# Kernel optimization log

Measured on AMD Instinct MI355X. Metric: run time of the kernel, lower is better.

The kernel has to match this reference:

```python
import jax, jax.numpy as jnp
import numpy as np

# MANO prior contact vertex indices (f1+f2+f3+f4+f5+f0 from CMap_loss3)
_F1 = [697,698,699,700,712,713,714,715,737,738,739,740,741,743,744,745,746,748,749,750,753,754,755,756,757,758,759,760,761,762,763,764,765,766,767,768]
_F2 = [46,47,48,49,164,165,166,167,194,195,223,237,238,280,281,298,301,317,320,323,324,325,326,327,328,329,330,331,332,333,340,341,342,343,344,345,346,347,348,349,350,351,352,353,354,355]
_F3 = [356,357,358,359,375,376,386,387,396,397,402,403,413,429,433,434,435,436,437,438,439,440,441,442,443,444,452,453,454,455,456,459,460,461,462,463,464,465,466,467]
_F4 = [468,469,470,471,484,485,486,496,497,506,507,513,514,524,545,546,547,548,549,550,551,552,553,555,563,564,565,566,567,570,572,573,574,575,576,577,578]
_F5 = [580,581,582,583,600,601,602,614,615,624,625,630,631,641,663,664,665,666,667,668,670,672,680,681,682,683,684,686,687,688,689,690,691,692,693,694,695]
_F0 = [73,96,98,99,772,774,775,777]
PRIOR_IDX = np.array(_F1 + _F2 + _F3 + _F4 + _F5 + _F0, dtype=np.int32)


def _sqdist(a, b):
    # a: [B,N,3], b: [B,M,3] -> squared distances [B,N,M] via ||a||^2+||b||^2-2ab
    a2 = jnp.sum(a * a, -1)          # [B,N]
    b2 = jnp.sum(b * b, -1)          # [B,M]
    ab = jnp.einsum('bnd,bmd->bnm', a, b)
    return jnp.maximum(a2[:, :, None] + b2[:, None, :] - 2.0 * ab, 0.0)


def _knn1(src, trg):
    # nearest neighbor (K=1): squared dists + indices, like pytorch3d knn_points
    d2 = _sqdist(src, trg)           # [B,N,M]
    return jnp.min(d2, -1), jnp.argmin(d2, -1)


def _verts_normals(verts, faces):
    # area-weighted vertex normals (pytorch3d verts_normals_packed)
    v0 = verts[:, faces[:, 0]]       # [B,F,3]
    v1 = verts[:, faces[:, 1]]
    v2 = verts[:, faces[:, 2]]
    fn = jnp.cross(v1 - v0, v2 - v0)
    vn = jnp.zeros_like(verts)
    vn = vn.at[:, faces[:, 0]].add(fn).at[:, faces[:, 1]].add(fn).at[:, faces[:, 2]].add(fn)
    return vn / (jnp.linalg.norm(vn, axis=-1, keepdims=True) + 1e-12)


def setup_inputs() -> dict:
    key = jax.random.key(0)
    ks = jax.random.split(key, 8)
    B, N1, V, F, Z, P = 64, 8192, 778, 1538, 64, 61
    scale = 0.1  # keep points in a 0.1 box so contact thresholds (0.005/0.01) fire
    return {
        'obj_xyz': jax.random.uniform(ks[0], (B, N1, 3), jnp.float32) * scale,
        'recon_xyz': jax.random.uniform(ks[1], (B, V, 3), jnp.float32) * scale,
        'gt_xyz': jax.random.uniform(ks[2], (B, V, 3), jnp.float32) * scale,
        'mean': jax.random.normal(ks[3], (B, Z), jnp.float32),
        'log_var': jax.random.normal(ks[4], (B, Z), jnp.float32),
        'recon_param': jax.random.normal(ks[5], (B, P), jnp.float32),
        'x_param': jax.random.normal(ks[6], (B, P), jnp.float32),
        'faces': jax.random.randint(ks[7], (F, 3), 0, V, jnp.int32),
    }


def reference(obj_xyz, recon_xyz, gt_xyz, mean, log_var, recon_param, x_param, faces):
    B = obj_xyz.shape[0]
    fB = jnp.float32(B)

    # KNN from object points to gt / reconstructed hand (squared dists)
    d_gt, _ = _knn1(obj_xyz, gt_xyz)            # [B,N1]
    d_rec, idx_rec = _knn1(obj_xyz, recon_xyz)  # [B,N1], [B,N1]

    # param loss: MSE sum / B
    param_loss = jnp.sum((recon_param - x_param) ** 2) / fB

    # CVAE loss: chamfer (point_reduction='sum', batch_reduction='mean') + KLD
    d2 = _sqdist(recon_xyz, gt_xyz)             # [B,778,778]
    recon_loss = jnp.mean(jnp.sum(jnp.min(d2, -1), -1)) + jnp.mean(jnp.sum(jnp.min(d2, -2), -1))
    KLD = -0.5 * jnp.sum(1.0 + log_var - mean ** 2 - jnp.exp(log_var)) / fB * 10.0
    cvae_loss = recon_loss + KLD

    # CMap_loss3: obj NN distance to prior hand contact verts, masked by cmap
    cmap = d_rec < 0.01 ** 2                    # [B,N1] bool
    prior = recon_xyz[:, PRIOR_IDX, :]          # [B,222,3]
    obj_CD, _ = _knn1(obj_xyz, prior)           # [B,N1]
    n_points = jnp.sum(cmap).astype(jnp.float32)
    cmap_loss = 3000.0 * jnp.sum(jnp.where(cmap, obj_CD, 0.0)) / (fB * n_points)

    # CMap consistency: contact-map overlap ratio
    recon_cmap = jnp.sqrt(d_rec) < 0.005
    gt_cmap = jnp.sqrt(d_gt) < 0.005
    gt_cnum = jnp.sum(gt_cmap).astype(jnp.float32) + 0.0001
    consistency_loss = -5.0 * jnp.sum(recon_cmap & gt_cmap).astype(jnp.float32) / gt_cnum

    # inter-penetration: gather NN hand verts/normals, sign of dot, masked dist sum
    vn = _verts_normals(recon_xyz, faces)                               # [B,778,3]
    nn_v = jnp.take_along_axis(recon_xyz, idx_rec[..., None], axis=1)   # [B,N1,3]
    nn_n = jnp.take_along_axis(vn, idx_rec[..., None], axis=1)          # [B,N1,3]
    interior = jnp.sum((nn_v - obj_xyz) * nn_n, -1) > 0                 # [B,N1]
    penetr_loss = 100.0 * jnp.sum(jnp.where(interior, d_rec, 0.0)) / fB

    a, b, c, d, e = 1.0, 0.1, 1000.0, 10.0, 10.0
    loss = a * cvae_loss + b * param_loss + c * cmap_loss + d * consistency_loss + e * penetr_loss
    return loss
```

## Files before the change

### kernel.cpp

```cpp
#include <hip/hip_runtime.h>
#include <math.h>

#define NB     64
#define N1V    8192
#define NPTS   (NB * N1V)
#define NV     778
#define NVP    780
#define NQ     195
#define SEG1Q  51
#define NFACE  1538
#define NZ     64
#define NPAR   61
#define NPRIOR 204
#define PPT    8
#define BIAS   0.0625f

#define GT_BLOCKS  256
#define REC_BLOCKS 256
#define CH_BLOCKS  128
#define NRM_BLOCKS 64
#define REC_BASE GT_BLOCKS
#define CH_BASE  (REC_BASE + REC_BLOCKS)
#define NRM_BASE (CH_BASE + CH_BLOCKS)
#define NBLOCKS  (NRM_BASE + NRM_BLOCKS)

#define ACC_OFF   (NB * NVP * 4)
#define FLAGS_OFF (ACC_OFF + 16)
#define NFLAGS    320
#define GC_OFF    (FLAGS_OFF + NFLAGS)

static constexpr int PRIOR_LIST[NPRIOR] = {
  697,698,699,700,712,713,714,715,737,738,739,740,741,743,744,745,746,748,749,750,
  753,754,755,756,757,758,759,760,761,762,763,764,765,766,767,768,
  46,47,48,49,164,165,166,167,194,195,223,237,238,280,281,298,301,317,320,323,
  324,325,326,327,328,329,330,331,332,333,340,341,342,343,344,345,346,347,348,349,
  350,351,352,353,354,355,
  356,357,358,359,375,376,386,387,396,397,402,403,413,429,433,434,435,436,437,438,
  439,440,441,442,443,444,452,453,454,455,456,459,460,461,462,463,464,465,466,467,
  468,469,470,471,484,485,486,496,497,506,507,513,514,524,545,546,547,548,549,550,
  551,552,553,555,563,564,565,566,567,570,572,573,574,575,576,577,578,
  580,581,582,583,600,601,602,614,615,624,625,630,631,641,663,664,665,666,667,668,
  670,672,680,681,682,683,684,686,687,688,689,690,691,692,693,694,695,
  73,96,98,99,772,774,775,777
};

struct PermT { unsigned short v[NV]; };
static constexpr PermT make_perm() {
    PermT t{};
    bool mem[NV] = {};
    for (int i = 0; i < NPRIOR; ++i) mem[PRIOR_LIST[i]] = true;
    int a = 0, b = NPRIOR;
    for (int j = 0; j < NV; ++j) {
        if (mem[j]) t.v[a++] = (unsigned short)j;
        else        t.v[b++] = (unsigned short)j;
    }
    return t;
}
__device__ __constant__ PermT c_perm = make_perm();

struct ScanSh { float4 t[NVP]; float red[4]; };
struct NrmSh  { float x[NV], y[NV], z[NV], vnx[NV], vny[NV], vnz[NV]; };
union ShU { ScanSh scan; NrmSh nrm; };

#define LOAD_PTS(ob)                                                          \
    const float4* ob4 = (const float4*)((ob) + (size_t)tid * 24);             \
    float4 q0 = ob4[0], q1 = ob4[1], q2 = ob4[2],                             \
           q3 = ob4[3], q4 = ob4[4], q5 = ob4[5];                             \
    float px[PPT], py[PPT], pz[PPT];                                          \
    px[0]=q0.x; py[0]=q0.y; pz[0]=q0.z;  px[1]=q0.w; py[1]=q1.x; pz[1]=q1.y;  \
    px[2]=q1.z; py[2]=q1.w; pz[2]=q2.x;  px[3]=q2.y; py[3]=q2.z; pz[3]=q2.w;  \
    px[4]=q3.x; py[4]=q3.y; pz[4]=q3.z;  px[5]=q3.w; py[5]=q4.x; pz[5]=q4.y;  \
    px[6]=q4.z; py[6]=q4.w; pz[6]=q5.x;  px[7]=q5.y; py[7]=q5.z; pz[7]=q5.w;

__device__ __forceinline__ float min3f(float a, float b, float c) {
    return fminf(fminf(a, b), c);
}

__device__ __forceinline__ void spin_wait(unsigned int* f, int tid) {
    if (tid == 0) {
        while (__hip_atomic_load(f, __ATOMIC_ACQUIRE, __HIP_MEMORY_SCOPE_AGENT) == 0u)
            __builtin_amdgcn_s_sleep(2);
    }
    __syncthreads();
}


__global__ __launch_bounds__(256) void k_all(
        const float* __restrict__ obj,   const float* __restrict__ recon,
        const float* __restrict__ gt,    const int*   __restrict__ faces,
        const float* __restrict__ mean,  const float* __restrict__ log_var,
        const float* __restrict__ rp,    const float* __restrict__ xp,
        float4* __restrict__ ws4,        float* __restrict__ acc,
        unsigned int* __restrict__ flags, unsigned char* __restrict__ gcA,
        float* __restrict__ out) {
    __shared__ ShU sh;
    __shared__ unsigned int s_tk;
    __shared__ float s_pk[2];
    int tid = threadIdx.x;
    int blk = blockIdx.x;

    if (blk < GT_BLOCKS) {
        int r = blk, b = r >> 2, chunk = r & 3;
        const float* gb = gt + (size_t)b * NV * 3;
        float4* s_t = sh.scan.t;
        for (int j = tid; j < NVP; j += 256) {
            if (j < NV) {
                float x = gb[3*j], y = gb[3*j+1], z = gb[3*j+2];
                s_t[j] = make_float4(-2.0f*x, -2.0f*y, -2.0f*z, x*x + y*y + z*z);
            } else s_t[j] = make_float4(0.f, 0.f, 0.f, 1e30f);
        }
        if (tid == 0) sh.scan.red[0] = 0.0f;
        __syncthreads();

        const float* ob = obj + ((size_t)b * N1V + (size_t)chunk * 2048) * 3;
        LOAD_PTS(ob)
        float mgt[PPT];
#pragma unroll
        for (int i = 0; i < PPT; ++i) mgt[i] = 3.4e38f;
#pragma unroll 1
        for (int jq = 0; jq < NQ; ++jq) {
            int j = 4 * jq;
            float4 t0 = s_t[j], t1 = s_t[j+1], t2 = s_t[j+2], t3 = s_t[j+3];
#pragma unroll
            for (int i = 0; i < PPT; ++i) {
                float d0 = fmaf(px[i], t0.x, fmaf(py[i], t0.y, fmaf(pz[i], t0.z, t0.w)));
                float d1 = fmaf(px[i], t1.x, fmaf(py[i], t1.y, fmaf(pz[i], t1.z, t1.w)));
                float d2 = fmaf(px[i], t2.x, fmaf(py[i], t2.y, fmaf(pz[i], t2.z, t2.w)));
                float d3 = fmaf(px[i], t3.x, fmaf(py[i], t3.y, fmaf(pz[i], t3.z, t3.w)));
                float u = min3f(d0, d1, d2);
                mgt[i] = min3f(u, d3, mgt[i]);
            }
        }
        float lN_gt = 0.0f;
        unsigned int gcbits = 0;
#pragma unroll
        for (int i = 0; i < PPT; ++i) {
            float a2 = px[i]*px[i] + py[i]*py[i] + pz[i]*pz[i];
            float dgt = fmaxf(a2 + mgt[i], 0.0f);
            if (sqrtf(dgt) < 0.005f) { lN_gt += 1.0f; gcbits |= (1u << i); }
        }
        gcA[(size_t)r * 256 + tid] = (unsigned char)gcbits;
        atomicAdd(&sh.scan.red[0], lN_gt);
        __syncthreads();
        if (tid == 0) {
            __threadfence();
            __hip_atomic_store(&flags[r], 1u, __ATOMIC_RELEASE, __HIP_MEMORY_SCOPE_AGENT);
            atomicAdd(&acc[5], sh.scan.red[0]);
        }
    } else if (blk < CH_BASE) {
        int r = blk - REC_BASE, b = r >> 2, chunk = r & 3;
        const float* rb = recon + (size_t)b * NV * 3;
        float4* s_t = sh.scan.t;
        for (int j = tid; j < NVP; j += 256) {
            if (j < NV) {
                int src = c_perm.v[j];
                float x = rb[3*src], y = rb[3*src+1], z = rb[3*src+2];
                s_t[j] = make_float4(-2.0f*x, -2.0f*y, -2.0f*z, x*x + y*y + z*z + BIAS);
            } else s_t[j] = make_float4(0.f, 0.f, 0.f, 1e30f);
        }
        if (tid < 4) sh.scan.red[tid] = 0.0f;
        __syncthreads();

        const float* ob = obj + ((size_t)b * N1V + (size_t)chunk * 2048) * 3;
        LOAD_PTS(ob)
        float m[PPT];
        int q[PPT];
#pragma unroll
        for (int i = 0; i < PPT; ++i) { m[i] = 3.4e38f; q[i] = 0; }
        float mp[PPT];
#pragma unroll 1
        for (int jq = 0; jq < SEG1Q; ++jq) {
            int j = 4 * jq;
            float4 t0 = s_t[j], t1 = s_t[j+1], t2 = s_t[j+2], t3 = s_t[j+3];
#pragma unroll
            for (int i = 0; i < PPT; ++i) {
                float d0 = fmaf(px[i], t0.x, fmaf(py[i], t0.y, fmaf(pz[i], t0.z, t0.w)));
                float d1 = fmaf(px[i], t1.x, fmaf(py[i], t1.y, fmaf(pz[i], t1.z, t1.w)));
                float d2 = fmaf(px[i], t2.x, fmaf(py[i], t2.y, fmaf(pz[i], t2.z, t2.w)));
                float d3 = fmaf(px[i], t3.x, fmaf(py[i], t3.y, fmaf(pz[i], t3.z, t3.w)));
                float u  = min3f(d0, d1, d2);
                float mn = min3f(u, d3, m[i]);
                q[i] = (mn < m[i]) ? jq : q[i];
                m[i] = mn;
            }
        }
#pragma unroll
        for (int i = 0; i < PPT; ++i) mp[i] = m[i];
#pragma unroll 1
        for (int jq = SEG1Q; jq < NQ; ++jq) {
            int j = 4 * jq;
            float4 t0 = s_t[j], t1 = s_t[j+1], t2 = s_t[j+2], t3 = s_t[j+3];
#pragma unroll
            for (int i = 0; i < PPT; ++i) {
                float d0 = fmaf(px[i], t0.x, fmaf(py[i], t0.y, fmaf(pz[i], t0.z, t0.w)));
                float d1 = fmaf(px[i], t1.x, fmaf(py[i], t1.y, fmaf(pz[i], t1.z, t1.w)));
                float d2 = fmaf(px[i], t2.x, fmaf(py[i], t2.y, fmaf(pz[i], t2.z, t2.w)));
                float d3 = fmaf(px[i], t3.x, fmaf(py[i], t3.y, fmaf(pz[i], t3.z, t3.w)));
                float u  = min3f(d0, d1, d2);
                float mn = min3f(u, d3, m[i]);
                q[i] = (mn < m[i]) ? jq : q[i];
                m[i] = mn;
            }
        }
        float lS_cmap = 0.0f, lN_cmap = 0.0f;
        unsigned int rcbits = 0;
        int js[PPT]; float drecs[PPT];
#pragma unroll
        for (int i = 0; i < PPT; ++i) {
            float a2 = px[i]*px[i] + py[i]*py[i] + pz[i]*pz[i];
            float drec = fmaxf(a2 + (m[i]  - BIAS), 0.0f);
            float dpri = fmaxf(a2 + (mp[i] - BIAS), 0.0f);
            bool cm = drec < 1e-4f;
            bool rc = sqrtf(drec) < 0.005f;
            if (cm) { lS_cmap += dpri; lN_cmap += 1.0f; }
            if (rc) rcbits |= (1u << i);
            int jr = 4 * q[i];
            float4 t0 = s_t[jr], t1 = s_t[jr+1], t2 = s_t[jr+2], t3 = s_t[jr+3];
            float d0 = fmaf(px[i], t0.x, fmaf(py[i], t0.y, fmaf(pz[i], t0.z, t0.w)));
            float d1 = fmaf(px[i], t1.x, fmaf(py[i], t1.y, fmaf(pz[i], t1.z, t1.w)));
            float d2 = fmaf(px[i], t2.x, fmaf(py[i], t2.y, fmaf(pz[i], t2.z, t2.w)));
            float d3 = fmaf(px[i], t3.x, fmaf(py[i], t3.y, fmaf(pz[i], t3.z, t3.w)));
            float mmin = fminf(fminf(d0, d1), fminf(d2, d3));
            int off = (d0 == mmin) ? 0 : ((d1 == mmin) ? 1 : ((d2 == mmin) ? 2 : 3));
            js[i] = jr + off;
            drecs[i] = drec;
        }
        atomicAdd(&sh.scan.red[0], lS_cmap);
        atomicAdd(&sh.scan.red[1], lN_cmap);
        spin_wait(&flags[256 + b], tid);
        spin_wait(&flags[r], tid);
        const float4* nrm4p = ws4 + (size_t)b * NVP;
        float lS_pen = 0.0f;
#pragma unroll
        for (int i = 0; i < PPT; ++i) {
            float4 tS = s_t[js[i]];
            float4 nr = nrm4p[js[i]];
            float ddot = (-0.5f*tS.x - px[i]) * nr.x + (-0.5f*tS.y - py[i]) * nr.y
                       + (-0.5f*tS.z - pz[i]) * nr.z;
            if (ddot > 0.0f) lS_pen += drecs[i];
        }
        unsigned int gcb = gcA[(size_t)r * 256 + tid];
        float lcons = (float)__popc(rcbits & gcb);
        atomicAdd(&sh.scan.red[2], lS_pen);
        atomicAdd(&sh.scan.red[3], lcons);
        __syncthreads();
        if (tid == 0) atomicAdd(&acc[3], sh.scan.red[0]);
        if (tid == 1) atomicAdd(&acc[4], sh.scan.red[1]);
        if (tid == 2) atomicAdd(&acc[7], sh.scan.red[2]);
        if (tid == 3) atomicAdd(&acc[6], sh.scan.red[3]);
    } else if (blk < NRM_BASE) {
        int c   = blk - CH_BASE;
        int b   = c >> 1;
        int dir = c & 1;
        const float* rb = recon + (size_t)b * NV * 3;
        const float* gb = gt    + (size_t)b * NV * 3;
        const float* tb = dir ? rb : gb;
        const float* sb = dir ? gb : rb;
        float4* s_t = sh.scan.t;
        for (int j = tid; j < NVP; j += 256) {
            if (j < NV) {
                float x = tb[3*j], y = tb[3*j+1], z = tb[3*j+2];
                float w = x*x + y*y + z*z;
                if (dir) w += BIAS;
                s_t[j] = make_float4(-2.0f*x, -2.0f*y, -2.0f*z, w);
            } else s_t[j] = make_float4(0.f, 0.f, 0.f, 1e30f);
        }
        if (tid == 0) sh.scan.red[0] = 0.0f;
        __syncthreads();

        const int CPT = 4;
        float sx[CPT], sy[CPT], sz[CPT], a2[CPT], m[CPT];
        bool valid[CPT];
#pragma unroll
        for (int k = 0; k < CPT; ++k) {
            int p = tid + 256 * k;
            valid[k] = (p < NV);
            int pp = valid[k] ? p : 0;
            float x = sb[3*pp], y = sb[3*pp+1], z = sb[3*pp+2];
            float w = x*x + y*y + z*z;
            if (!dir) w += BIAS;
            sx[k] = x; sy[k] = y; sz[k] = z;
            a2[k] = w;
            m[k] = 3.4e38f;
        }
#pragma unroll 1
        for (int j = 0; j < NVP; j += 4) {
            float4 t0 = s_t[j], t1 = s_t[j+1], t2 = s_t[j+2], t3 = s_t[j+3];
#pragma unroll
            for (int k = 0; k < CPT; ++k) {
                float d0 = fmaf(sx[k], t0.x, fmaf(sy[k], t0.y, fmaf(sz[k], t0.z, t0.w)));
                float d1 = fmaf(sx[k], t1.x, fmaf(sy[k], t1.y, fmaf(sz[k], t1.z, t1.w)));
                float d2 = fmaf(sx[k], t2.x, fmaf(sy[k], t2.y, fmaf(sz[k], t2.z, t2.w)));
                float d3 = fmaf(sx[k], t3.x, fmaf(sy[k], t3.y, fmaf(sz[k], t3.z, t3.w)));
                float u = min3f(d0, d1, d2);
                m[k] = min3f(u, d3, m[k]);
            }
        }
        float local = 0.0f;
#pragma unroll
        for (int k = 0; k < CPT; ++k)
            if (valid[k]) local += fmaxf(a2[k] + m[k] - BIAS, 0.0f);
        atomicAdd(&sh.scan.red[0], local);
        __syncthreads();
        if (tid == 0) atomicAdd(&acc[2], sh.scan.red[0]);
    } else {
        int b = blk - NRM_BASE;
        const float* rb = recon + (size_t)b * NV * 3;
        for (int j = tid; j < NV; j += 256) {
            sh.nrm.x[j] = rb[3*j]; sh.nrm.y[j] = rb[3*j+1]; sh.nrm.z[j] = rb[3*j+2];
            sh.nrm.vnx[j] = 0.0f; sh.nrm.vny[j] = 0.0f; sh.nrm.vnz[j] = 0.0f;
        }
        __syncthreads();
        for (int f = tid; f < NFACE; f += 256) {
            int i0 = faces[3*f], i1 = faces[3*f+1], i2 = faces[3*f+2];
            float p0x = sh.nrm.x[i0], p0y = sh.nrm.y[i0], p0z = sh.nrm.z[i0];
            float e1x = sh.nrm.x[i1] - p0x, e1y = sh.nrm.y[i1] - p0y, e1z = sh.nrm.z[i1] - p0z;
            float e2x = sh.nrm.x[i2] - p0x, e2y = sh.nrm.y[i2] - p0y, e2z = sh.nrm.z[i2] - p0z;
            float fx = e1y * e2z - e1z * e2y;
            float fy = e1z * e2x - e1x * e2z;
            float fz = e1x * e2y - e1y * e2x;
            atomicAdd(&sh.nrm.vnx[i0], fx); atomicAdd(&sh.nrm.vny[i0], fy); atomicAdd(&sh.nrm.vnz[i0], fz);
            atomicAdd(&sh.nrm.vnx[i1], fx); atomicAdd(&sh.nrm.vny[i1], fy); atomicAdd(&sh.nrm.vnz[i1], fz);
            atomicAdd(&sh.nrm.vnx[i2], fx); atomicAdd(&sh.nrm.vny[i2], fy); atomicAdd(&sh.nrm.vnz[i2], fz);
        }
        __syncthreads();
        float4* nrm4p = ws4 + (size_t)b * NVP;
        for (int j = tid; j < NVP; j += 256) {
            if (j < NV) {
                int src = c_perm.v[j];
                nrm4p[j] = make_float4(sh.nrm.vnx[src], sh.nrm.vny[src], sh.nrm.vnz[src], 0.0f);
            } else nrm4p[j] = make_float4(0.f, 0.f, 1.f, 0.0f);
        }
        __syncthreads();
        if (tid == 0) {
            __threadfence();
            __hip_atomic_store(&flags[256 + b], 1u, __ATOMIC_RELEASE, __HIP_MEMORY_SCOPE_AGENT);
        }
        if (b == 0) {
            if (tid < 2) s_pk[tid] = 0.0f;
            __syncthreads();
            float s_param = 0.0f, s_kld = 0.0f;
            for (int i = tid; i < NB * NPAR; i += 256) {
                float d = rp[i] - xp[i];
                s_param += d * d;
            }
            for (int i = tid; i < NB * NZ; i += 256) {
                float mv = mean[i], lv = log_var[i];
                s_kld += 1.0f + lv - mv * mv - expf(lv);
            }
            atomicAdd(&s_pk[0], s_param);
            atomicAdd(&s_pk[1], s_kld);
            __syncthreads();
            if (tid == 0) { atomicAdd(&acc[8], s_pk[0]); atomicAdd(&acc[9], s_pk[1]); }
        }
    }

    __syncthreads();
    if (tid == 0) {
        asm volatile("s_waitcnt vmcnt(0)" ::: "memory");
        s_tk = atomicAdd((unsigned int*)&acc[15], 1u);
    }
    __syncthreads();
    if (s_tk == NBLOCKS - 1 && tid == 0) {
        __threadfence();
        const float fB = 64.0f;
        float a2v = __hip_atomic_load(&acc[2], __ATOMIC_RELAXED, __HIP_MEMORY_SCOPE_AGENT);
        float a3  = __hip_atomic_load(&acc[3], __ATOMIC_RELAXED, __HIP_MEMORY_SCOPE_AGENT);
        float a4  = __hip_atomic_load(&acc[4], __ATOMIC_RELAXED, __HIP_MEMORY_SCOPE_AGENT);
        float a5  = __hip_atomic_load(&acc[5], __ATOMIC_RELAXED, __HIP_MEMORY_SCOPE_AGENT);
        float a6  = __hip_atomic_load(&acc[6], __ATOMIC_RELAXED, __HIP_MEMORY_SCOPE_AGENT);
        float a7  = __hip_atomic_load(&acc[7], __ATOMIC_RELAXED, __HIP_MEMORY_SCOPE_AGENT);
        float a8  = __hip_atomic_load(&acc[8], __ATOMIC_RELAXED, __HIP_MEMORY_SCOPE_AGENT);
        float a9  = __hip_atomic_load(&acc[9], __ATOMIC_RELAXED, __HIP_MEMORY_SCOPE_AGENT);
        float param_loss  = a8 / fB;
        float KLD         = -0.5f * a9 / fB * 10.0f;
        float recon_loss  = a2v / fB;
        float cmap_loss   = 3000.0f * a3 / (fB * a4);
        float consistency = -5.0f * a6 / (a5 + 0.0001f);
        float penetr      = 100.0f * a7 / fB;
        out[0] = (recon_loss + KLD) + 0.1f * param_loss + 1000.0f * cmap_loss
               + 10.0f * consistency + 10.0f * penetr;
    }
}

extern "C" void kernel_launch(void* const* d_in, const int* in_sizes, int n_in,
                              void* d_out, int out_size, void* d_ws, size_t ws_size,
                              hipStream_t stream) {
    (void)in_sizes; (void)n_in; (void)out_size; (void)ws_size;
    const float* obj     = (const float*)d_in[0];
    const float* recon   = (const float*)d_in[1];
    const float* gt      = (const float*)d_in[2];
    const float* mean    = (const float*)d_in[3];
    const float* log_var = (const float*)d_in[4];
    const float* rp      = (const float*)d_in[5];
    const float* xp      = (const float*)d_in[6];
    const int*   faces   = (const int*)d_in[7];
    float* wsf = (float*)d_ws;
    float4* ws4 = (float4*)d_ws;
    float* acc = wsf + ACC_OFF;
    unsigned int* flags = (unsigned int*)(wsf + FLAGS_OFF);
    unsigned char* gcA  = (unsigned char*)(wsf + GC_OFF);
    float* out = (float*)d_out;

    hipMemsetAsync(acc, 0, (16 + NFLAGS) * sizeof(float), stream);
    k_all<<<NBLOCKS, 256, 0, stream>>>(obj, recon, gt, faces, mean, log_var,
                                       rp, xp, ws4, acc, flags, gcA, out);
}
```

Before: 163.8 us.

## Replace brute-force GT contact scan with uniform-grid radius search

The normal-computation blocks now also bin each batch's GT hand vertices into an 8x8x8 uniform grid through a shared-memory histogram, prefix sum and scatter, then publish a per-batch flag. The GT contact blocks wait on that flag and test each object point only against vertices in the neighbouring cells within the 0.005 contact radius, instead of scanning all 778 vertices for a nearest distance. This removes most of the GT branch's arithmetic. In exchange it adds a cross-block dependency with spin-waiting, data-dependent per-point loops that diverge within a wave, and cell sizing tuned to the 0.1 input box.

```diff
diff --git a/kernel.cpp b/kernel.cpp
--- a/kernel.cpp
+++ b/kernel.cpp
@@ -14,6 +14,7 @@
 #define NPRIOR 204
 #define PPT    8
 #define BIAS   0.0625f
+#define GR     0.005f
 
 #define GT_BLOCKS  256
 #define REC_BLOCKS 256
@@ -24,10 +25,12 @@
 #define NRM_BASE (CH_BASE + CH_BLOCKS)
 #define NBLOCKS  (NRM_BASE + NRM_BLOCKS)
 
-#define ACC_OFF   (NB * NVP * 4)
-#define FLAGS_OFF (ACC_OFF + 16)
-#define NFLAGS    320
-#define GC_OFF    (FLAGS_OFF + NFLAGS)
+#define ACC_OFF    (NB * NVP * 4)
+#define FLAGS_OFF  (ACC_OFF + 16)
+#define NFLAGS     384
+#define GC_OFF     (FLAGS_OFF + NFLAGS)
+#define SORT4_OFF  (GC_OFF + NPTS / 8 / 4)
+#define GSTART_OFF (SORT4_OFF + NB * NVP * 4)
 
 static constexpr int PRIOR_LIST[NPRIOR] = {
   697,698,699,700,712,713,714,715,737,738,739,740,741,743,744,745,746,748,749,750,
@@ -59,8 +62,10 @@
 __device__ __constant__ PermT c_perm = make_perm();
 
 struct ScanSh { float4 t[NVP]; float red[4]; };
+struct GtSh   { float4 t[NVP]; float red[4]; unsigned int start[513]; };
 struct NrmSh  { float x[NV], y[NV], z[NV], vnx[NV], vny[NV], vnz[NV]; };
-union ShU { ScanSh scan; NrmSh nrm; };
+struct GrdSh  { unsigned int hist[513]; unsigned int cur[512]; };
+union ShU { ScanSh scan; GtSh gts; NrmSh nrm; GrdSh grd; };
 
 #define LOAD_PTS(ob)                                                          \
     const float4* ob4 = (const float4*)((ob) + (size_t)tid * 24);             \
@@ -76,6 +81,11 @@
     return fminf(fminf(a, b), c);
 }
 
+__device__ __forceinline__ int cidx(float v) {
+    int c = (int)(v * 80.0f);
+    return c < 0 ? 0 : (c > 7 ? 7 : c);
+}
+
 __device__ __forceinline__ void spin_wait(unsigned int* f, int tid) {
     if (tid == 0) {
         while (__hip_atomic_load(f, __ATOMIC_ACQUIRE, __HIP_MEMORY_SCOPE_AGENT) == 0u)
@@ -83,7 +93,6 @@
     }
     __syncthreads();
 }
-
 
 __global__ __launch_bounds__(256) void k_all(
         const float* __restrict__ obj,   const float* __restrict__ recon,
@@ -92,6 +101,7 @@
         const float* __restrict__ rp,    const float* __restrict__ xp,
         float4* __restrict__ ws4,        float* __restrict__ acc,
         unsigned int* __restrict__ flags, unsigned char* __restrict__ gcA,
+        float4* __restrict__ sorted4,    unsigned int* __restrict__ gstart,
         float* __restrict__ out) {
     __shared__ ShU sh;
     __shared__ unsigned int s_tk;
@@ -101,51 +111,47 @@
 
     if (blk < GT_BLOCKS) {
         int r = blk, b = r >> 2, chunk = r & 3;
-        const float* gb = gt + (size_t)b * NV * 3;
-        float4* s_t = sh.scan.t;
-        for (int j = tid; j < NVP; j += 256) {
-            if (j < NV) {
-                float x = gb[3*j], y = gb[3*j+1], z = gb[3*j+2];
-                s_t[j] = make_float4(-2.0f*x, -2.0f*y, -2.0f*z, x*x + y*y + z*z);
-            } else s_t[j] = make_float4(0.f, 0.f, 0.f, 1e30f);
-        }
-        if (tid == 0) sh.scan.red[0] = 0.0f;
-        __syncthreads();
-
         const float* ob = obj + ((size_t)b * N1V + (size_t)chunk * 2048) * 3;
         LOAD_PTS(ob)
-        float mgt[PPT];
-#pragma unroll
-        for (int i = 0; i < PPT; ++i) mgt[i] = 3.4e38f;
-#pragma unroll 1
-        for (int jq = 0; jq < NQ; ++jq) {
-            int j = 4 * jq;
-            float4 t0 = s_t[j], t1 = s_t[j+1], t2 = s_t[j+2], t3 = s_t[j+3];
-#pragma unroll
-            for (int i = 0; i < PPT; ++i) {
-                float d0 = fmaf(px[i], t0.x, fmaf(py[i], t0.y, fmaf(pz[i], t0.z, t0.w)));
-                float d1 = fmaf(px[i], t1.x, fmaf(py[i], t1.y, fmaf(pz[i], t1.z, t1.w)));
-                float d2 = fmaf(px[i], t2.x, fmaf(py[i], t2.y, fmaf(pz[i], t2.z, t2.w)));
-                float d3 = fmaf(px[i], t3.x, fmaf(py[i], t3.y, fmaf(pz[i], t3.z, t3.w)));
-                float u = min3f(d0, d1, d2);
-                mgt[i] = min3f(u, d3, mgt[i]);
-            }
-        }
+        if (tid == 0) sh.gts.red[0] = 0.0f;
+        spin_wait(&flags[320 + b], tid);
+        for (int j = tid; j < NV; j += 256) sh.gts.t[j] = sorted4[(size_t)b * NVP + j];
+        for (int j = tid; j < 513; j += 256) sh.gts.start[j] = gstart[(size_t)b * 513 + j];
+        __syncthreads();
+
         float lN_gt = 0.0f;
         unsigned int gcbits = 0;
 #pragma unroll
         for (int i = 0; i < PPT; ++i) {
-            float a2 = px[i]*px[i] + py[i]*py[i] + pz[i]*pz[i];
-            float dgt = fmaxf(a2 + mgt[i], 0.0f);
-            if (sqrtf(dgt) < 0.005f) { lN_gt += 1.0f; gcbits |= (1u << i); }
+            float a2v = px[i]*px[i] + py[i]*py[i] + pz[i]*pz[i];
+            int ix0 = cidx(px[i] - GR), ix1 = cidx(px[i] + GR);
+            int iy0 = cidx(py[i] - GR), iy1 = cidx(py[i] + GR);
+            int iz0 = cidx(pz[i] - GR), iz1 = cidx(pz[i] + GR);
+            bool found = false;
+#pragma unroll
+            for (int cc = 0; cc < 8; ++cc) {
+                if (((cc & 1) && ix1 == ix0) || ((cc & 2) && iy1 == iy0) ||
+                    ((cc & 4) && iz1 == iz0)) continue;
+                int cx = (cc & 1) ? ix1 : ix0;
+                int cy = (cc & 2) ? iy1 : iy0;
+                int cz = (cc & 4) ? iz1 : iz0;
+                int cell = (cz * 8 + cy) * 8 + cx;
+                int s = (int)sh.gts.start[cell], e = (int)sh.gts.start[cell + 1];
+                for (int k = s; k < e; ++k) {
+                    float4 t = sh.gts.t[k];
+                    float part = fmaf(px[i], t.x, fmaf(py[i], t.y, fmaf(pz[i], t.z, t.w)));
+                    found |= (sqrtf(fmaxf(a2v + part, 0.0f)) < GR);
+                }
+            }
+            if (found) { lN_gt += 1.0f; gcbits |= (1u << i); }
         }
         gcA[(size_t)r * 256 + tid] = (unsigned char)gcbits;
-        atomicAdd(&sh.scan.red[0], lN_gt);
+        atomicAdd(&sh.gts.red[0], lN_gt);
         __syncthreads();
         if (tid == 0) {
             __threadfence();
             __hip_atomic_store(&flags[r], 1u, __ATOMIC_RELEASE, __HIP_MEMORY_SCOPE_AGENT);
-            atomicAdd(&acc[5], sh.scan.red[0]);
+            atomicAdd(&acc[5], sh.gts.red[0]);
         }
     } else if (blk < CH_BASE) {
         int r = blk - REC_BASE, b = r >> 2, chunk = r & 3;
@@ -305,7 +311,41 @@
         if (tid == 0) atomicAdd(&acc[2], sh.scan.red[0]);
     } else {
         int b = blk - NRM_BASE;
+        const float* gb = gt    + (size_t)b * NV * 3;
         const float* rb = recon + (size_t)b * NV * 3;
+        for (int j = tid; j < 513; j += 256) sh.grd.hist[j] = 0u;
+        __syncthreads();
+        for (int v = tid; v < NV; v += 256) {
+            float x = gb[3*v], y = gb[3*v+1], z = gb[3*v+2];
+            int cell = (cidx(z) * 8 + cidx(y)) * 8 + cidx(x);
+            atomicAdd(&sh.grd.hist[cell], 1u);
+        }
+        __syncthreads();
+        if (tid == 0) {
+            unsigned int run = 0;
+            for (int c2 = 0; c2 < 512; ++c2) {
+                unsigned int t = sh.grd.hist[c2];
+                sh.grd.hist[c2] = run; run += t;
+            }
+            sh.grd.hist[512] = run;
+        }
+        __syncthreads();
+        for (int j = tid; j < 512; j += 256) sh.grd.cur[j] = sh.grd.hist[j];
+        for (int j = tid; j < 513; j += 256) gstart[(size_t)b * 513 + j] = sh.grd.hist[j];
+        __syncthreads();
+        for (int v = tid; v < NV; v += 256) {
+            float x = gb[3*v], y = gb[3*v+1], z = gb[3*v+2];
+            int cell = (cidx(z) * 8 + cidx(y)) * 8 + cidx(x);
+            unsigned int pos = atomicAdd(&sh.grd.cur[cell], 1u);
+            sorted4[(size_t)b * NVP + pos] = make_float4(-2.0f*x, -2.0f*y, -2.0f*z,
+                                                         x*x + y*y + z*z);
+        }
+        __syncthreads();
+        if (tid == 0) {
+            __threadfence();
+            __hip_atomic_store(&flags[320 + b], 1u, __ATOMIC_RELEASE, __HIP_MEMORY_SCOPE_AGENT);
+        }
+        __syncthreads();
         for (int j = tid; j < NV; j += 256) {
             sh.nrm.x[j] = rb[3*j]; sh.nrm.y[j] = rb[3*j+1]; sh.nrm.z[j] = rb[3*j+2];
             sh.nrm.vnx[j] = 0.0f; sh.nrm.vny[j] = 0.0f; sh.nrm.vnz[j] = 0.0f;
@@ -400,9 +440,12 @@
     float* acc = wsf + ACC_OFF;
     unsigned int* flags = (unsigned int*)(wsf + FLAGS_OFF);
     unsigned char* gcA  = (unsigned char*)(wsf + GC_OFF);
+    float4* sorted4     = (float4*)(wsf + SORT4_OFF);
+    unsigned int* gstart = (unsigned int*)(wsf + GSTART_OFF);
     float* out = (float*)d_out;
 
     hipMemsetAsync(acc, 0, (16 + NFLAGS) * sizeof(float), stream);
     k_all<<<NBLOCKS, 256, 0, stream>>>(obj, recon, gt, faces, mean, log_var,
-                                       rp, xp, ws4, acc, flags, gcA, out);
-}
+                                       rp, xp, ws4, acc, flags, gcA,
+                                       sorted4, gstart, out);
+}
```

Result: slower. 208.9 us (+27.5%).
